# Performance work log

Hardware: AMD Instinct MI355X
Metric: run time of the kernel (lower is better)

## Reference

```python
import jax, jax.numpy as jnp
import numpy as np

IOU_THRESHOLDS = (0.5, 0.75)
B, N, G = 256, 4000, 50


def _iou(amin, amax, bmin, bmax):
    # broadcasted temporal IoU: anchors [N,1] vs boxes [1,G] -> [N,G]
    inter = jnp.maximum(jnp.minimum(amax, bmax) - jnp.maximum(amin, bmin), 0.0)
    union = (amax - amin) + (bmax - bmin) - inter
    return inter / union


def _greedy_tp(segments, gts, thr):
    # segments: [N,2], gts: [G,2]. Replicates AP.get_values greedy matching:
    # for each label (in order), claim the first (lowest-index) unused proposal
    # whose IoU > thr. Final used-mask == is_TP.
    ious = _iou(segments[:, 0:1], segments[:, 1:2], gts[None, :, 0], gts[None, :, 1])  # [N,G]
    pot = ious > thr
    n = segments.shape[0]

    def step(used, col):  # col: [N] bool, candidates for this label
        cand = col & ~used
        idx = jnp.argmax(cand)  # first True (argmax of bool is first max)
        used = jnp.where(jnp.any(cand), used.at[idx].set(True), used)
        return used, None

    used, _ = jax.lax.scan(step, jnp.zeros((n,), jnp.bool_), pot.T)
    return used  # [N] bool


def _ap_for_threshold(scores, segments, labels, thr):
    is_tp = jax.vmap(lambda s, g: _greedy_tp(s, g, thr))(segments, labels)  # [B,N]
    conf = scores.reshape(-1)                       # [B*N]
    tp = is_tp.reshape(-1).astype(jnp.float32)
    order = jnp.argsort(-conf)                      # sort by confidence, descending
    tp = tp[order]
    n_labels = labels.shape[0] * labels.shape[1]
    m = tp.shape[0]
    acc_tp = jnp.cumsum(tp)
    precision = acc_tp / (jnp.arange(m, dtype=jnp.float32) + 1.0)
    recall = acc_tp / jnp.float32(n_labels)
    # curve = [[1,0]] then (recall, precision) reversed; AP = sum(|dx| * cummax(y)[:-1])
    x = jnp.concatenate([jnp.ones((1,), jnp.float32), recall[::-1]])
    y = jnp.concatenate([jnp.zeros((1,), jnp.float32), precision[::-1]])
    y_max = jax.lax.cummax(y, axis=0)
    x_diff = jnp.abs(jnp.diff(x))
    return jnp.sum(x_diff * y_max[:-1])


def setup_inputs() -> dict:
    key = jax.random.key(0)
    k1, k2, k3, k4, k5 = jax.random.split(key, 5)
    scores = jax.random.uniform(k1, (B, N), dtype=jnp.float32)
    p_start = jax.random.uniform(k2, (B, N), dtype=jnp.float32) * 0.9
    p_len = jax.random.uniform(k3, (B, N), dtype=jnp.float32) * 0.1 + 0.005
    segments = jnp.stack([p_start, p_start + p_len], axis=-1)  # [B,N,2], start<end
    g_start = jax.random.uniform(k4, (B, G), dtype=jnp.float32) * 0.9
    g_len = jax.random.uniform(k5, (B, G), dtype=jnp.float32) * 0.1 + 0.005
    labels = jnp.stack([g_start, g_start + g_len], axis=-1)    # [B,G,2]
    return {"scores": scores, "segments": segments, "labels": labels}


def reference(scores, segments, labels):
    # returns AP at each IoU threshold, shape [len(IOU_THRESHOLDS)]
    return jnp.stack([_ap_for_threshold(scores, segments, labels, t) for t in IOU_THRESHOLDS])
```

## Files before the change

kernel.cpp:

```cpp
#include <hip/hip_runtime.h>


#define B_ 256
#define N_ 4000
#define G_ 50
#define M_ (B_ * N_)
#define NL_ (B_ * G_)
#define NBKT 2048
#define KP 16
#define TILE (NL_ / KP)

#define M0_ 0x1.000001p-1
#define M1_ 0x1.800001p-1

typedef unsigned long long u64;

__device__ __forceinline__ unsigned bucket_of(float c) {
    unsigned b = (unsigned)(c * 2048.0f);
    return b > (NBKT - 1) ? (NBKT - 1) : b;
}

__global__ __launch_bounds__(1024) void tp_kernel(
    const float* __restrict__ seg,
    const float* __restrict__ gts,
    const float* __restrict__ conf,
    int* __restrict__ tpIdx,
    int* __restrict__ cnt,
    unsigned short* __restrict__ pbh)
{
    const int tid  = threadIdx.x;
    const int lane = tid & 63;
    const int wv   = tid >> 6;
    const int b    = blockIdx.x;

    __shared__ float2 gtl[G_];
    __shared__ u64 cand[2][G_][64];
    __shared__ unsigned hls[NBKT];
    __shared__ int lcnt[2];

    #pragma unroll
    for (int k = 0; k < NBKT / 1024; ++k) hls[k * 1024 + tid] = 0u;
    if (tid < G_) gtl[tid] = ((const float2*)gts)[b * G_ + tid];
    if (tid < 2) lcnt[tid] = 0;
    __syncthreads();

    const float* cb = conf + (size_t)b * N_;
    #pragma unroll
    for (int s = 0; s < 4; ++s) {
        int n = s * 1024 + tid;
        if (n < N_) atomicAdd(&hls[bucket_of(cb[n])], 1u);
    }

    const float2* sb = (const float2*)(seg + (size_t)b * (N_ * 2));
    float pmin[4], pmax[4], plen[4];
    #pragma unroll
    for (int s = 0; s < 4; ++s) {
        int n = s * 1024 + tid;
        if (n < N_) { float2 v = sb[n]; pmin[s] = v.x; pmax[s] = v.y; }
        else { pmin[s] = 1e9f; pmax[s] = 1e9f; }
        plen[s] = pmax[s] - pmin[s];
    }
    for (int g = 0; g < G_; ++g) {
        float2 gt = gtl[g];
        float glen = gt.y - gt.x;
        u64 m0[4], m1[4];
        #pragma unroll
        for (int s = 0; s < 4; ++s) {
            float inter = fmaxf(fminf(pmax[s], gt.y) - fmaxf(pmin[s], gt.x), 0.0f);
            float uni = plen[s] + glen - inter;
            double di = (double)inter;
            double du = (double)uni;
            m0[s] = __ballot(di > M0_ * du);
            m1[s] = __ballot(di > M1_ * du);
        }
        if (lane == 0) {
            #pragma unroll
            for (int s = 0; s < 4; ++s) {
                cand[0][g][s * 16 + wv] = m0[s];
                cand[1][g][s * 16 + wv] = m1[s];
            }
        }
    }
    __syncthreads();

    #pragma unroll
    for (int k = 0; k < NBKT / 1024; ++k) {
        int bin = k * 1024 + tid;
        pbh[(size_t)b * NBKT + bin] = (unsigned short)hls[bin];
    }

    if (wv < 2) {
        const int thr_i = wv;
        u64 used = 0ull;
        for (int g = 0; g < G_; ++g) {
            u64 c = cand[thr_i][g][lane] & ~used;
            u64 ball = __ballot(c != 0ull);
            if (ball) {
                int fl = __ffsll(ball) - 1;
                if (lane == fl) used |= (c & (0ull - c));
            }
        }
        int cpop = __popcll(used);
        if (cpop) {
            int j = atomicAdd(&lcnt[thr_i], cpop);
            u64 u = used;
            while (u) {
                int bit = __ffsll(u) - 1;
                u &= u - 1;
                tpIdx[thr_i * NL_ + b * G_ + j++] = b * N_ + lane * 64 + bit;
            }
        }
    }
    __syncthreads();
    if (tid < 2) cnt[tid * B_ + b] = lcnt[tid];
}

__global__ __launch_bounds__(256) void s1_kernel(
    unsigned short* __restrict__ pbh,
    unsigned* __restrict__ total)
{
    __shared__ unsigned sc[256];
    const int bin = blockIdx.x;
    const int b = threadIdx.x;
    unsigned v = pbh[(size_t)b * NBKT + bin];
    sc[b] = v;
    __syncthreads();
    for (int off = 1; off < 256; off <<= 1) {
        unsigned add = (b >= off) ? sc[b - off] : 0u;
        __syncthreads();
        sc[b] += add;
        __syncthreads();
    }
    pbh[(size_t)b * NBKT + bin] = (unsigned short)(sc[b] - v);
    if (b == 255) total[bin] = sc[255];
}

__global__ __launch_bounds__(1024) void s2_kernel(
    const unsigned* __restrict__ total, unsigned* __restrict__ binStart)
{
    __shared__ unsigned part[1024];
    int t = threadIdx.x;
    uint2 v2 = ((const uint2*)total)[t];
    unsigned s = v2.x + v2.y;
    part[t] = s;
    __syncthreads();
    for (int off = 1; off < 1024; off <<= 1) {
        unsigned add = (t >= off) ? part[t - off] : 0u;
        __syncthreads();
        part[t] += add;
        __syncthreads();
    }
    unsigned base = (t == 0) ? 0u : part[t - 1];
    ((uint2*)binStart)[t] = make_uint2(base, base + v2.x);
}

__global__ __launch_bounds__(1024) void scatter_kernel(
    const float* __restrict__ conf,
    const unsigned short* __restrict__ pbh,
    const unsigned* __restrict__ binStart,
    u64* __restrict__ sKey)
{
    __shared__ unsigned baseB[NBKT];
    __shared__ unsigned lofs[NBKT];
    const int tid = threadIdx.x;
    const int b = blockIdx.x;
    #pragma unroll
    for (int k = 0; k < NBKT / 1024; ++k) {
        int bin = k * 1024 + tid;
        baseB[bin] = binStart[bin] + pbh[(size_t)b * NBKT + bin];
        lofs[bin] = 0u;
    }
    __syncthreads();
    const float* cb = conf + (size_t)b * N_;
    #pragma unroll
    for (int s = 0; s < 4; ++s) {
        int n = s * 1024 + tid;
        if (n < N_) {
            float c = cb[n];
            unsigned bin = bucket_of(c);
            unsigned lo = atomicAdd(&lofs[bin], 1u);
            unsigned idx = (unsigned)(b * N_ + n);
            sKey[baseB[bin] + lo] = ((u64)__float_as_uint(c) << 32) | (u64)(0xFFFFFFFFu - idx);
        }
    }
}

__global__ __launch_bounds__(256) void rank_kernel(
    const float* __restrict__ conf,
    const int* __restrict__ tpIdx,
    const int* __restrict__ cnt,
    const unsigned* __restrict__ total,
    const unsigned* __restrict__ binStart,
    const u64* __restrict__ sKey,
    int* __restrict__ tpRank)
{
    const int lane = threadIdx.x & 63;
    const int w = (blockIdx.x << 2) | (threadIdx.x >> 6);
    if (w >= 2 * NL_) return;
    const int thr_i = w / NL_;
    const int t = w - thr_i * NL_;
    const int batch = t / G_;
    const int j = t - batch * G_;

    if (j < cnt[thr_i * B_ + batch]) {
        int e = tpIdx[thr_i * NL_ + t];
        float c = conf[e];
        u64 keyE = ((u64)__float_as_uint(c) << 32) | (u64)(0xFFFFFFFFu - (unsigned)e);
        unsigned bin = bucket_of(c);
        unsigned lo = binStart[bin], n = total[bin];
        int r = M_ - (int)lo - (int)n;
        for (unsigned base = 0; base < n; base += 64) {
            unsigned k = base + lane;
            bool pred = (k < n) && (sKey[lo + k] > keyE);
            r += (int)__popcll(__ballot(pred));
        }
        if (lane == 0) tpRank[thr_i * NL_ + t] = r;
    } else {
        if (lane == 0) tpRank[thr_i * NL_ + t] = M_ + t;
    }
}

__global__ __launch_bounds__(256) void pos1_kernel(
    const int* __restrict__ tpRank,
    int* __restrict__ pcount)
{
    __shared__ alignas(16) int tile[TILE];
    const int k = blockIdx.y, thr_i = blockIdx.z;
    const int* base = tpRank + thr_i * NL_;
    for (int i = threadIdx.x; i < TILE; i += 256)
        tile[i] = base[k * TILE + i];
    __syncthreads();

    const int t0 = blockIdx.x * 1024 + threadIdx.x;
    int r[4], c[4] = {0, 0, 0, 0};
    #pragma unroll
    for (int j = 0; j < 4; ++j) {
        int t = t0 + j * 256;
        r[j] = (t < NL_) ? base[t] : -1;
    }
    const int4* l4 = (const int4*)tile;
    #pragma unroll 4
    for (int i = 0; i < TILE / 4; ++i) {
        int4 v = l4[i];
        #pragma unroll
        for (int j = 0; j < 4; ++j)
            c[j] += (v.x < r[j]) + (v.y < r[j]) + (v.z < r[j]) + (v.w < r[j]);
    }
    #pragma unroll
    for (int j = 0; j < 4; ++j) {
        int t = t0 + j * 256;
        if (t < NL_) pcount[(thr_i * KP + k) * NL_ + t] = c[j];
    }
}

__global__ __launch_bounds__(1024) void ap_kernel(
    const int* __restrict__ tpRank,
    const int* __restrict__ pcount,
    float* __restrict__ out)
{
    const int C = 13;
    __shared__ int sr[NL_];
    __shared__ float cmax[1024];
    __shared__ double red[1024];
    int thr_i = blockIdx.x;
    int t = threadIdx.x;

    #pragma unroll
    for (int j = 0; j < C; ++j) {
        int tt = t + j * 1024;
        if (tt < NL_) {
            int p = 0;
            #pragma unroll
            for (int k = 0; k < KP; ++k)
                p += pcount[(thr_i * KP + k) * NL_ + tt];
            sr[p] = tpRank[thr_i * NL_ + tt];
        }
    }
    __syncthreads();

    float pr[C]; int rk[C];
    #pragma unroll
    for (int k = 0; k < C; ++k) {
        int i = t * C + k;
        rk[k] = (i < NL_) ? sr[i] : 0x7FFFFFFF;
        pr[k] = (rk[k] < M_) ? (float)(i + 1) / (float)(rk[k] + 1) : -1.0f;
    }
    float suf[C];
    float run = -1.0f;
    #pragma unroll
    for (int k = C - 1; k >= 0; --k) { run = fmaxf(run, pr[k]); suf[k] = run; }

    cmax[t] = run;
    __syncthreads();
    for (int off = 1; off < 1024; off <<= 1) {
        float v = cmax[t];
        float o = (t + off < 1024) ? cmax[t + off] : -1.0f;
        __syncthreads();
        cmax[t] = fmaxf(v, o);
        __syncthreads();
    }
    float follow = (t + 1 < 1024) ? cmax[t + 1] : -1.0f;

    double acc = 0.0;
    #pragma unroll
    for (int k = 0; k < C; ++k) {
        int i = t * C + k;
        if (rk[k] >= 1 && rk[k] < M_) {
            float smax = fmaxf(suf[k], follow);
            float rhi = (float)(i + 1) / 12800.0f;
            float rlo = (float)i / 12800.0f;
            acc += (double)((rhi - rlo) * smax);
        }
    }
    red[t] = acc;
    __syncthreads();
    for (int off = 512; off >= 1; off >>= 1) {
        if (t < off) red[t] += red[t + off];
        __syncthreads();
    }
    if (t == 0) out[thr_i] = (float)red[0];
}

extern "C" void kernel_launch(void* const* d_in, const int* in_sizes, int n_in,
                              void* d_out, int out_size, void* d_ws, size_t ws_size,
                              hipStream_t stream) {
    const float* scores = (const float*)d_in[0];
    const float* seg    = (const float*)d_in[1];
    const float* gts    = (const float*)d_in[2];
    float* out = (float*)d_out;

    char* p = (char*)d_ws;
    int*            cnt        = (int*)p;             p += 4096;
    int*            tpIdx      = (int*)p;             p += 2 * NL_ * 4;
    int*            tpRank     = (int*)p;             p += 2 * NL_ * 4;
    unsigned*       total      = (unsigned*)p;        p += NBKT * 4;
    unsigned*       binStart   = (unsigned*)p;        p += NBKT * 4;
    unsigned short* pbh        = (unsigned short*)p;  p += (size_t)B_ * NBKT * 2;
    u64*            sKey       = (u64*)p;             p += (size_t)M_ * 8;
    int*            pcount     = (int*)sKey;
    (void)ws_size; (void)in_sizes; (void)n_in; (void)out_size;

    tp_kernel<<<B_, 1024, 0, stream>>>(seg, gts, scores, tpIdx, cnt, pbh);
    s1_kernel<<<NBKT, 256, 0, stream>>>(pbh, total);
    s2_kernel<<<1, 1024, 0, stream>>>(total, binStart);
    scatter_kernel<<<B_, 1024, 0, stream>>>(scores, pbh, binStart, sKey);
    rank_kernel<<<(2 * NL_ + 3) / 4, 256, 0, stream>>>(scores, tpIdx, cnt,
                                                       total, binStart, sKey, tpRank);
    pos1_kernel<<<dim3(13, KP, 2), 256, 0, stream>>>(tpRank, pcount);
    ap_kernel<<<2, 1024, 0, stream>>>(tpRank, pcount, out);
}
```

Before: 187.6 us.

## Fuse the seven-kernel pipeline into one cooperative kernel with grid syncs

Merges the TP-matching, histogram scan, bin-start scan, scatter, rank, position-count and AP kernels into a single cooperative mega-kernel. Grid-wide barriers replace the kernel boundaries, and shared memory is reused across phases through a union. Each block now recomputes the small bin-start scan locally instead of waiting on a separate single-block launch. This removes per-launch overhead and inter-kernel gaps. In exchange, the grid is fixed at 256 blocks of 1024 threads, so the rank and position phases loop over work with less parallelism, the position phase leaves most threads idle, and every phase pays grid.sync costs.

```diff
diff --git a/kernel.cpp b/kernel.cpp
--- a/kernel.cpp
+++ b/kernel.cpp
@@ -1,4 +1,5 @@
 #include <hip/hip_runtime.h>
+#include <hip/hip_cooperative_groups.h>
 
 
 #define B_ 256
@@ -14,311 +15,294 @@
 #define M1_ 0x1.800001p-1
 
 typedef unsigned long long u64;
+namespace cg = cooperative_groups;
 
 __device__ __forceinline__ unsigned bucket_of(float c) {
     unsigned b = (unsigned)(c * 2048.0f);
     return b > (NBKT - 1) ? (NBKT - 1) : b;
 }
 
-__global__ __launch_bounds__(1024) void tp_kernel(
-    const float* __restrict__ seg,
-    const float* __restrict__ gts,
+union SharedU {
+    struct { float2 gtl[G_]; u64 cand[2][G_][64]; unsigned hls[NBKT]; int lcnt[2]; } tp;
+    struct { unsigned sc[4][256]; } s1;
+    struct { unsigned part[1024]; unsigned baseB[NBKT]; unsigned lofs[NBKT]; } sca;
+    struct { int tile[TILE]; } pos;
+    struct { int sr[NL_]; float cmax[1024]; double red[1024]; } ap;
+};
+
+__global__ __launch_bounds__(1024, 4) void mega_kernel(
+    const float* __restrict__ seg, const float* __restrict__ gts,
     const float* __restrict__ conf,
-    int* __restrict__ tpIdx,
-    int* __restrict__ cnt,
-    unsigned short* __restrict__ pbh)
+    int* __restrict__ tpIdx, int* __restrict__ cnt,
+    unsigned short* __restrict__ pbh,
+    unsigned* __restrict__ total, unsigned* __restrict__ binStart,
+    u64* __restrict__ sKey, int* __restrict__ tpRank,
+    int* __restrict__ pcount, float* __restrict__ out)
 {
-    const int tid  = threadIdx.x;
-    const int lane = tid & 63;
-    const int wv   = tid >> 6;
-    const int b    = blockIdx.x;
-
-    __shared__ float2 gtl[G_];
-    __shared__ u64 cand[2][G_][64];
-    __shared__ unsigned hls[NBKT];
-    __shared__ int lcnt[2];
-
-    #pragma unroll
-    for (int k = 0; k < NBKT / 1024; ++k) hls[k * 1024 + tid] = 0u;
-    if (tid < G_) gtl[tid] = ((const float2*)gts)[b * G_ + tid];
-    if (tid < 2) lcnt[tid] = 0;
-    __syncthreads();
-
-    const float* cb = conf + (size_t)b * N_;
-    #pragma unroll
-    for (int s = 0; s < 4; ++s) {
-        int n = s * 1024 + tid;
-        if (n < N_) atomicAdd(&hls[bucket_of(cb[n])], 1u);
-    }
-
-    const float2* sb = (const float2*)(seg + (size_t)b * (N_ * 2));
-    float pmin[4], pmax[4], plen[4];
-    #pragma unroll
-    for (int s = 0; s < 4; ++s) {
-        int n = s * 1024 + tid;
-        if (n < N_) { float2 v = sb[n]; pmin[s] = v.x; pmax[s] = v.y; }
-        else { pmin[s] = 1e9f; pmax[s] = 1e9f; }
-        plen[s] = pmax[s] - pmin[s];
-    }
-    for (int g = 0; g < G_; ++g) {
-        float2 gt = gtl[g];
-        float glen = gt.y - gt.x;
-        u64 m0[4], m1[4];
+    cg::grid_group grid = cg::this_grid();
+    __shared__ SharedU sh;
+    const int tid = threadIdx.x, lane = tid & 63, wv = tid >> 6;
+    const int blk = blockIdx.x;
+
+    {
+        const int b = blk;
+        #pragma unroll
+        for (int k = 0; k < NBKT / 1024; ++k) sh.tp.hls[k * 1024 + tid] = 0u;
+        if (tid < G_) sh.tp.gtl[tid] = ((const float2*)gts)[b * G_ + tid];
+        if (tid < 2) sh.tp.lcnt[tid] = 0;
+        __syncthreads();
+
+        const float* cb = conf + (size_t)b * N_;
         #pragma unroll
         for (int s = 0; s < 4; ++s) {
-            float inter = fmaxf(fminf(pmax[s], gt.y) - fmaxf(pmin[s], gt.x), 0.0f);
-            float uni = plen[s] + glen - inter;
-            double di = (double)inter;
-            double du = (double)uni;
-            m0[s] = __ballot(di > M0_ * du);
-            m1[s] = __ballot(di > M1_ * du);
-        }
-        if (lane == 0) {
+            int n = s * 1024 + tid;
+            if (n < N_) atomicAdd(&sh.tp.hls[bucket_of(cb[n])], 1u);
+        }
+
+        const float2* sb = (const float2*)(seg + (size_t)b * (N_ * 2));
+        float pmin[4], pmax[4], plen[4];
+        #pragma unroll
+        for (int s = 0; s < 4; ++s) {
+            int n = s * 1024 + tid;
+            if (n < N_) { float2 v = sb[n]; pmin[s] = v.x; pmax[s] = v.y; }
+            else { pmin[s] = 1e9f; pmax[s] = 1e9f; }
+            plen[s] = pmax[s] - pmin[s];
+        }
+        for (int g = 0; g < G_; ++g) {
+            float2 gt = sh.tp.gtl[g];
+            float glen = gt.y - gt.x;
+            u64 m0[4], m1[4];
             #pragma unroll
             for (int s = 0; s < 4; ++s) {
-                cand[0][g][s * 16 + wv] = m0[s];
-                cand[1][g][s * 16 + wv] = m1[s];
-            }
-        }
-    }
-    __syncthreads();
-
-    #pragma unroll
-    for (int k = 0; k < NBKT / 1024; ++k) {
-        int bin = k * 1024 + tid;
-        pbh[(size_t)b * NBKT + bin] = (unsigned short)hls[bin];
-    }
-
-    if (wv < 2) {
-        const int thr_i = wv;
-        u64 used = 0ull;
-        for (int g = 0; g < G_; ++g) {
-            u64 c = cand[thr_i][g][lane] & ~used;
-            u64 ball = __ballot(c != 0ull);
-            if (ball) {
-                int fl = __ffsll(ball) - 1;
-                if (lane == fl) used |= (c & (0ull - c));
-            }
-        }
-        int cpop = __popcll(used);
-        if (cpop) {
-            int j = atomicAdd(&lcnt[thr_i], cpop);
-            u64 u = used;
-            while (u) {
-                int bit = __ffsll(u) - 1;
-                u &= u - 1;
-                tpIdx[thr_i * NL_ + b * G_ + j++] = b * N_ + lane * 64 + bit;
-            }
-        }
-    }
-    __syncthreads();
-    if (tid < 2) cnt[tid * B_ + b] = lcnt[tid];
-}
-
-__global__ __launch_bounds__(256) void s1_kernel(
-    unsigned short* __restrict__ pbh,
-    unsigned* __restrict__ total)
-{
-    __shared__ unsigned sc[256];
-    const int bin = blockIdx.x;
-    const int b = threadIdx.x;
-    unsigned v = pbh[(size_t)b * NBKT + bin];
-    sc[b] = v;
-    __syncthreads();
-    for (int off = 1; off < 256; off <<= 1) {
-        unsigned add = (b >= off) ? sc[b - off] : 0u;
-        __syncthreads();
-        sc[b] += add;
-        __syncthreads();
-    }
-    pbh[(size_t)b * NBKT + bin] = (unsigned short)(sc[b] - v);
-    if (b == 255) total[bin] = sc[255];
-}
-
-__global__ __launch_bounds__(1024) void s2_kernel(
-    const unsigned* __restrict__ total, unsigned* __restrict__ binStart)
-{
-    __shared__ unsigned part[1024];
-    int t = threadIdx.x;
-    uint2 v2 = ((const uint2*)total)[t];
-    unsigned s = v2.x + v2.y;
-    part[t] = s;
-    __syncthreads();
-    for (int off = 1; off < 1024; off <<= 1) {
-        unsigned add = (t >= off) ? part[t - off] : 0u;
-        __syncthreads();
-        part[t] += add;
-        __syncthreads();
-    }
-    unsigned base = (t == 0) ? 0u : part[t - 1];
-    ((uint2*)binStart)[t] = make_uint2(base, base + v2.x);
-}
-
-__global__ __launch_bounds__(1024) void scatter_kernel(
-    const float* __restrict__ conf,
-    const unsigned short* __restrict__ pbh,
-    const unsigned* __restrict__ binStart,
-    u64* __restrict__ sKey)
-{
-    __shared__ unsigned baseB[NBKT];
-    __shared__ unsigned lofs[NBKT];
-    const int tid = threadIdx.x;
-    const int b = blockIdx.x;
-    #pragma unroll
-    for (int k = 0; k < NBKT / 1024; ++k) {
-        int bin = k * 1024 + tid;
-        baseB[bin] = binStart[bin] + pbh[(size_t)b * NBKT + bin];
-        lofs[bin] = 0u;
-    }
-    __syncthreads();
-    const float* cb = conf + (size_t)b * N_;
-    #pragma unroll
-    for (int s = 0; s < 4; ++s) {
-        int n = s * 1024 + tid;
-        if (n < N_) {
-            float c = cb[n];
-            unsigned bin = bucket_of(c);
-            unsigned lo = atomicAdd(&lofs[bin], 1u);
-            unsigned idx = (unsigned)(b * N_ + n);
-            sKey[baseB[bin] + lo] = ((u64)__float_as_uint(c) << 32) | (u64)(0xFFFFFFFFu - idx);
-        }
-    }
-}
-
-__global__ __launch_bounds__(256) void rank_kernel(
-    const float* __restrict__ conf,
-    const int* __restrict__ tpIdx,
-    const int* __restrict__ cnt,
-    const unsigned* __restrict__ total,
-    const unsigned* __restrict__ binStart,
-    const u64* __restrict__ sKey,
-    int* __restrict__ tpRank)
-{
-    const int lane = threadIdx.x & 63;
-    const int w = (blockIdx.x << 2) | (threadIdx.x >> 6);
-    if (w >= 2 * NL_) return;
-    const int thr_i = w / NL_;
-    const int t = w - thr_i * NL_;
-    const int batch = t / G_;
-    const int j = t - batch * G_;
-
-    if (j < cnt[thr_i * B_ + batch]) {
-        int e = tpIdx[thr_i * NL_ + t];
-        float c = conf[e];
-        u64 keyE = ((u64)__float_as_uint(c) << 32) | (u64)(0xFFFFFFFFu - (unsigned)e);
-        unsigned bin = bucket_of(c);
-        unsigned lo = binStart[bin], n = total[bin];
-        int r = M_ - (int)lo - (int)n;
-        for (unsigned base = 0; base < n; base += 64) {
-            unsigned k = base + lane;
-            bool pred = (k < n) && (sKey[lo + k] > keyE);
-            r += (int)__popcll(__ballot(pred));
-        }
-        if (lane == 0) tpRank[thr_i * NL_ + t] = r;
-    } else {
-        if (lane == 0) tpRank[thr_i * NL_ + t] = M_ + t;
-    }
-}
-
-__global__ __launch_bounds__(256) void pos1_kernel(
-    const int* __restrict__ tpRank,
-    int* __restrict__ pcount)
-{
-    __shared__ alignas(16) int tile[TILE];
-    const int k = blockIdx.y, thr_i = blockIdx.z;
-    const int* base = tpRank + thr_i * NL_;
-    for (int i = threadIdx.x; i < TILE; i += 256)
-        tile[i] = base[k * TILE + i];
-    __syncthreads();
-
-    const int t0 = blockIdx.x * 1024 + threadIdx.x;
-    int r[4], c[4] = {0, 0, 0, 0};
-    #pragma unroll
-    for (int j = 0; j < 4; ++j) {
-        int t = t0 + j * 256;
-        r[j] = (t < NL_) ? base[t] : -1;
-    }
-    const int4* l4 = (const int4*)tile;
-    #pragma unroll 4
-    for (int i = 0; i < TILE / 4; ++i) {
-        int4 v = l4[i];
-        #pragma unroll
-        for (int j = 0; j < 4; ++j)
-            c[j] += (v.x < r[j]) + (v.y < r[j]) + (v.z < r[j]) + (v.w < r[j]);
-    }
-    #pragma unroll
-    for (int j = 0; j < 4; ++j) {
-        int t = t0 + j * 256;
-        if (t < NL_) pcount[(thr_i * KP + k) * NL_ + t] = c[j];
-    }
-}
-
-__global__ __launch_bounds__(1024) void ap_kernel(
-    const int* __restrict__ tpRank,
-    const int* __restrict__ pcount,
-    float* __restrict__ out)
-{
-    const int C = 13;
-    __shared__ int sr[NL_];
-    __shared__ float cmax[1024];
-    __shared__ double red[1024];
-    int thr_i = blockIdx.x;
-    int t = threadIdx.x;
-
-    #pragma unroll
-    for (int j = 0; j < C; ++j) {
-        int tt = t + j * 1024;
-        if (tt < NL_) {
-            int p = 0;
-            #pragma unroll
-            for (int k = 0; k < KP; ++k)
-                p += pcount[(thr_i * KP + k) * NL_ + tt];
-            sr[p] = tpRank[thr_i * NL_ + tt];
-        }
-    }
-    __syncthreads();
-
-    float pr[C]; int rk[C];
-    #pragma unroll
-    for (int k = 0; k < C; ++k) {
-        int i = t * C + k;
-        rk[k] = (i < NL_) ? sr[i] : 0x7FFFFFFF;
-        pr[k] = (rk[k] < M_) ? (float)(i + 1) / (float)(rk[k] + 1) : -1.0f;
-    }
-    float suf[C];
-    float run = -1.0f;
-    #pragma unroll
-    for (int k = C - 1; k >= 0; --k) { run = fmaxf(run, pr[k]); suf[k] = run; }
-
-    cmax[t] = run;
-    __syncthreads();
-    for (int off = 1; off < 1024; off <<= 1) {
-        float v = cmax[t];
-        float o = (t + off < 1024) ? cmax[t + off] : -1.0f;
-        __syncthreads();
-        cmax[t] = fmaxf(v, o);
-        __syncthreads();
-    }
-    float follow = (t + 1 < 1024) ? cmax[t + 1] : -1.0f;
-
-    double acc = 0.0;
-    #pragma unroll
-    for (int k = 0; k < C; ++k) {
-        int i = t * C + k;
-        if (rk[k] >= 1 && rk[k] < M_) {
-            float smax = fmaxf(suf[k], follow);
-            float rhi = (float)(i + 1) / 12800.0f;
-            float rlo = (float)i / 12800.0f;
-            acc += (double)((rhi - rlo) * smax);
-        }
-    }
-    red[t] = acc;
-    __syncthreads();
-    for (int off = 512; off >= 1; off >>= 1) {
-        if (t < off) red[t] += red[t + off];
-        __syncthreads();
-    }
-    if (t == 0) out[thr_i] = (float)red[0];
+                float inter = fmaxf(fminf(pmax[s], gt.y) - fmaxf(pmin[s], gt.x), 0.0f);
+                float uni = plen[s] + glen - inter;
+                double di = (double)inter;
+                double du = (double)uni;
+                m0[s] = __ballot(di > M0_ * du);
+                m1[s] = __ballot(di > M1_ * du);
+            }
+            if (lane == 0) {
+                #pragma unroll
+                for (int s = 0; s < 4; ++s) {
+                    sh.tp.cand[0][g][s * 16 + wv] = m0[s];
+                    sh.tp.cand[1][g][s * 16 + wv] = m1[s];
+                }
+            }
+        }
+        __syncthreads();
+
+        #pragma unroll
+        for (int k = 0; k < NBKT / 1024; ++k) {
+            int bin = k * 1024 + tid;
+            pbh[(size_t)b * NBKT + bin] = (unsigned short)sh.tp.hls[bin];
+        }
+
+        if (wv < 2) {
+            const int thr_i = wv;
+            u64 used = 0ull;
+            for (int g = 0; g < G_; ++g) {
+                u64 c = sh.tp.cand[thr_i][g][lane] & ~used;
+                u64 ball = __ballot(c != 0ull);
+                if (ball) {
+                    int fl = __ffsll(ball) - 1;
+                    if (lane == fl) used |= (c & (0ull - c));
+                }
+            }
+            int cpop = __popcll(used);
+            if (cpop) {
+                int j = atomicAdd(&sh.tp.lcnt[thr_i], cpop);
+                u64 u = used;
+                while (u) {
+                    int bit = __ffsll(u) - 1;
+                    u &= u - 1;
+                    tpIdx[thr_i * NL_ + b * G_ + j++] = b * N_ + lane * 64 + bit;
+                }
+            }
+        }
+        __syncthreads();
+        if (tid < 2) cnt[tid * B_ + b] = sh.tp.lcnt[tid];
+    }
+    grid.sync();
+
+    {
+        const int grp = tid >> 8;
+        const int b = tid & 255;
+        for (int r = 0; r < 2; ++r) {
+            int bin = blk * 8 + r * 4 + grp;
+            unsigned v = pbh[(size_t)b * NBKT + bin];
+            sh.s1.sc[grp][b] = v;
+            __syncthreads();
+            for (int off = 1; off < 256; off <<= 1) {
+                unsigned add = (b >= off) ? sh.s1.sc[grp][b - off] : 0u;
+                __syncthreads();
+                sh.s1.sc[grp][b] += add;
+                __syncthreads();
+            }
+            pbh[(size_t)b * NBKT + bin] = (unsigned short)(sh.s1.sc[grp][b] - v);
+            if (b == 255) total[bin] = sh.s1.sc[grp][255];
+            __syncthreads();
+        }
+    }
+    grid.sync();
+
+    {
+        uint2 v2 = ((const uint2*)total)[tid];
+        unsigned s = v2.x + v2.y;
+        sh.sca.part[tid] = s;
+        __syncthreads();
+        for (int off = 1; off < 1024; off <<= 1) {
+            unsigned add = (tid >= off) ? sh.sca.part[tid - off] : 0u;
+            __syncthreads();
+            sh.sca.part[tid] += add;
+            __syncthreads();
+        }
+        unsigned base = tid ? sh.sca.part[tid - 1] : 0u;
+        if (blk == 0) ((uint2*)binStart)[tid] = make_uint2(base, base + v2.x);
+        const int b = blk;
+        sh.sca.baseB[2 * tid]     = base        + pbh[(size_t)b * NBKT + 2 * tid];
+        sh.sca.baseB[2 * tid + 1] = base + v2.x + pbh[(size_t)b * NBKT + 2 * tid + 1];
+        sh.sca.lofs[2 * tid] = 0u;
+        sh.sca.lofs[2 * tid + 1] = 0u;
+        __syncthreads();
+        const float* cb = conf + (size_t)b * N_;
+        #pragma unroll
+        for (int s4 = 0; s4 < 4; ++s4) {
+            int n = s4 * 1024 + tid;
+            if (n < N_) {
+                float c = cb[n];
+                unsigned bin = bucket_of(c);
+                unsigned lo = atomicAdd(&sh.sca.lofs[bin], 1u);
+                unsigned idx = (unsigned)(b * N_ + n);
+                sKey[sh.sca.baseB[bin] + lo] =
+                    ((u64)__float_as_uint(c) << 32) | (u64)(0xFFFFFFFFu - idx);
+            }
+        }
+    }
+    grid.sync();
+
+    {
+        const int gw = blk * 16 + wv;
+        for (int t = gw; t < 2 * NL_; t += 4096) {
+            const int thr_i = t / NL_;
+            const int tt = t - thr_i * NL_;
+            const int batch = tt / G_;
+            const int j = tt - batch * G_;
+            if (j < cnt[thr_i * B_ + batch]) {
+                int e = tpIdx[thr_i * NL_ + tt];
+                float c = conf[e];
+                u64 keyE = ((u64)__float_as_uint(c) << 32) | (u64)(0xFFFFFFFFu - (unsigned)e);
+                unsigned bin = bucket_of(c);
+                unsigned lo = binStart[bin], n = total[bin];
+                int r = M_ - (int)lo - (int)n;
+                for (unsigned base = 0; base < n; base += 64) {
+                    unsigned k = base + lane;
+                    bool pred = (k < n) && (sKey[lo + k] > keyE);
+                    r += (int)__popcll(__ballot(pred));
+                }
+                if (lane == 0) tpRank[thr_i * NL_ + tt] = r;
+            } else {
+                if (lane == 0) tpRank[thr_i * NL_ + tt] = M_ + t % NL_ + thr_i;
+            }
+        }
+    }
+    grid.sync();
+
+    {
+        for (int task = blk; task < 2 * KP * 13; task += B_) {
+            int xb = task % 13;
+            int rem = task / 13;
+            int k = rem % KP;
+            int thr_i = rem / KP;
+            const int* baseR = tpRank + thr_i * NL_;
+            for (int i = tid; i < TILE; i += 1024)
+                sh.pos.tile[i] = baseR[k * TILE + i];
+            __syncthreads();
+            if (tid < 256) {
+                const int t0 = xb * 1024 + tid;
+                int r[4], c[4] = {0, 0, 0, 0};
+                #pragma unroll
+                for (int j = 0; j < 4; ++j) {
+                    int t = t0 + j * 256;
+                    r[j] = (t < NL_) ? baseR[t] : -1;
+                }
+                const int4* l4 = (const int4*)sh.pos.tile;
+                #pragma unroll 4
+                for (int i = 0; i < TILE / 4; ++i) {
+                    int4 v = l4[i];
+                    #pragma unroll
+                    for (int j = 0; j < 4; ++j)
+                        c[j] += (v.x < r[j]) + (v.y < r[j]) + (v.z < r[j]) + (v.w < r[j]);
+                }
+                #pragma unroll
+                for (int j = 0; j < 4; ++j) {
+                    int t = t0 + j * 256;
+                    if (t < NL_) pcount[(thr_i * KP + k) * NL_ + t] = c[j];
+                }
+            }
+            __syncthreads();
+        }
+    }
+    grid.sync();
+
+    if (blk < 2) {
+        const int C = 13;
+        const int thr_i = blk;
+        const int t = tid;
+        #pragma unroll
+        for (int j = 0; j < C; ++j) {
+            int tt = t + j * 1024;
+            if (tt < NL_) {
+                int p = 0;
+                #pragma unroll
+                for (int k = 0; k < KP; ++k)
+                    p += pcount[(thr_i * KP + k) * NL_ + tt];
+                sh.ap.sr[p] = tpRank[thr_i * NL_ + tt];
+            }
+        }
+        __syncthreads();
+
+        float pr[C]; int rk[C];
+        #pragma unroll
+        for (int k = 0; k < C; ++k) {
+            int i = t * C + k;
+            rk[k] = (i < NL_) ? sh.ap.sr[i] : 0x7FFFFFFF;
+            pr[k] = (rk[k] < M_) ? (float)(i + 1) / (float)(rk[k] + 1) : -1.0f;
+        }
+        float suf[C];
+        float run = -1.0f;
+        #pragma unroll
+        for (int k = C - 1; k >= 0; --k) { run = fmaxf(run, pr[k]); suf[k] = run; }
+
+        sh.ap.cmax[t] = run;
+        __syncthreads();
+        for (int off = 1; off < 1024; off <<= 1) {
+            float v = sh.ap.cmax[t];
+            float o = (t + off < 1024) ? sh.ap.cmax[t + off] : -1.0f;
+            __syncthreads();
+            sh.ap.cmax[t] = fmaxf(v, o);
+            __syncthreads();
+        }
+        float follow = (t + 1 < 1024) ? sh.ap.cmax[t + 1] : -1.0f;
+
+        double acc = 0.0;
+        #pragma unroll
+        for (int k = 0; k < C; ++k) {
+            int i = t * C + k;
+            if (rk[k] >= 1 && rk[k] < M_) {
+                float smax = fmaxf(suf[k], follow);
+                float rhi = (float)(i + 1) / 12800.0f;
+                float rlo = (float)i / 12800.0f;
+                acc += (double)((rhi - rlo) * smax);
+            }
+        }
+        sh.ap.red[t] = acc;
+        __syncthreads();
+        for (int off = 512; off >= 1; off >>= 1) {
+            if (t < off) sh.ap.red[t] += sh.ap.red[t + off];
+            __syncthreads();
+        }
+        if (t == 0) out[thr_i] = (float)sh.ap.red[0];
+    }
 }
 
 extern "C" void kernel_launch(void* const* d_in, const int* in_sizes, int n_in,
@@ -340,12 +324,12 @@
     int*            pcount     = (int*)sKey;
     (void)ws_size; (void)in_sizes; (void)n_in; (void)out_size;
 
-    tp_kernel<<<B_, 1024, 0, stream>>>(seg, gts, scores, tpIdx, cnt, pbh);
-    s1_kernel<<<NBKT, 256, 0, stream>>>(pbh, total);
-    s2_kernel<<<1, 1024, 0, stream>>>(total, binStart);
-    scatter_kernel<<<B_, 1024, 0, stream>>>(scores, pbh, binStart, sKey);
-    rank_kernel<<<(2 * NL_ + 3) / 4, 256, 0, stream>>>(scores, tpIdx, cnt,
-                                                       total, binStart, sKey, tpRank);
-    pos1_kernel<<<dim3(13, KP, 2), 256, 0, stream>>>(tpRank, pcount);
-    ap_kernel<<<2, 1024, 0, stream>>>(tpRank, pcount, out);
+    void* args[] = {
+        (void*)&seg, (void*)&gts, (void*)&scores,
+        (void*)&tpIdx, (void*)&cnt, (void*)&pbh,
+        (void*)&total, (void*)&binStart,
+        (void*)&sKey, (void*)&tpRank, (void*)&pcount, (void*)&out
+    };
+    hipLaunchCooperativeKernel((const void*)mega_kernel, dim3(B_), dim3(1024),
+                               args, 0, stream);
 }
```

New measurement: 354.3 us. +88.9%, slower.

## Fold bin-start scan into scatter kernel and use wave shuffles in s1

Applied to the files above, without the earlier changes.

Removes the single-block s2 launch: each scatter block now recomputes the global exclusive scan of bucket totals in shared memory, and block 0 writes binStart for later kernels. The s1 per-bin scan across batches becomes a wave-level shuffle scan with four bins per block and four batches per lane, replacing the shared-memory scan with many barriers. KP is also halved, changing the tiling of pos1. This trades one kernel launch and a serial dependency for redundant scan work in every scatter block.

```diff
diff --git a/kernel.cpp b/kernel.cpp
--- a/kernel.cpp
+++ b/kernel.cpp
@@ -7,7 +7,7 @@
 #define M_ (B_ * N_)
 #define NL_ (B_ * G_)
 #define NBKT 2048
-#define KP 16
+#define KP 8
 #define TILE (NL_ / KP)
 
 #define M0_ 0x1.000001p-1
@@ -119,62 +119,62 @@
     unsigned short* __restrict__ pbh,
     unsigned* __restrict__ total)
 {
-    __shared__ unsigned sc[256];
-    const int bin = blockIdx.x;
-    const int b = threadIdx.x;
-    unsigned v = pbh[(size_t)b * NBKT + bin];
-    sc[b] = v;
-    __syncthreads();
-    for (int off = 1; off < 256; off <<= 1) {
-        unsigned add = (b >= off) ? sc[b - off] : 0u;
-        __syncthreads();
-        sc[b] += add;
-        __syncthreads();
-    }
-    pbh[(size_t)b * NBKT + bin] = (unsigned short)(sc[b] - v);
-    if (b == 255) total[bin] = sc[255];
-}
-
-__global__ __launch_bounds__(1024) void s2_kernel(
-    const unsigned* __restrict__ total, unsigned* __restrict__ binStart)
-{
-    __shared__ unsigned part[1024];
-    int t = threadIdx.x;
-    uint2 v2 = ((const uint2*)total)[t];
-    unsigned s = v2.x + v2.y;
-    part[t] = s;
-    __syncthreads();
-    for (int off = 1; off < 1024; off <<= 1) {
-        unsigned add = (t >= off) ? part[t - off] : 0u;
-        __syncthreads();
-        part[t] += add;
-        __syncthreads();
-    }
-    unsigned base = (t == 0) ? 0u : part[t - 1];
-    ((uint2*)binStart)[t] = make_uint2(base, base + v2.x);
+    const int lane = threadIdx.x & 63;
+    const int bin = blockIdx.x * 4 + (threadIdx.x >> 6);
+    unsigned v[4], loc[4], s = 0;
+    #pragma unroll
+    for (int i = 0; i < 4; ++i) {
+        v[i] = pbh[(size_t)(lane * 4 + i) * NBKT + bin];
+        loc[i] = s; s += v[i];
+    }
+    unsigned x = s;
+    #pragma unroll
+    for (int off = 1; off < 64; off <<= 1) {
+        unsigned t = __shfl_up(x, off, 64);
+        if (lane >= off) x += t;
+    }
+    unsigned excl = x - s;
+    #pragma unroll
+    for (int i = 0; i < 4; ++i)
+        pbh[(size_t)(lane * 4 + i) * NBKT + bin] = (unsigned short)(excl + loc[i]);
+    if (lane == 63) total[bin] = x;
 }
 
 __global__ __launch_bounds__(1024) void scatter_kernel(
     const float* __restrict__ conf,
     const unsigned short* __restrict__ pbh,
-    const unsigned* __restrict__ binStart,
+    const unsigned* __restrict__ total,
+    unsigned* __restrict__ binStart,
     u64* __restrict__ sKey)
 {
+    __shared__ unsigned part[1024];
     __shared__ unsigned baseB[NBKT];
     __shared__ unsigned lofs[NBKT];
     const int tid = threadIdx.x;
     const int b = blockIdx.x;
-    #pragma unroll
-    for (int k = 0; k < NBKT / 1024; ++k) {
-        int bin = k * 1024 + tid;
-        baseB[bin] = binStart[bin] + pbh[(size_t)b * NBKT + bin];
-        lofs[bin] = 0u;
-    }
-    __syncthreads();
+
+    uint2 v2 = ((const uint2*)total)[tid];
+    unsigned s = v2.x + v2.y;
+    part[tid] = s;
+    __syncthreads();
+    for (int off = 1; off < 1024; off <<= 1) {
+        unsigned add = (tid >= off) ? part[tid - off] : 0u;
+        __syncthreads();
+        part[tid] += add;
+        __syncthreads();
+    }
+    unsigned base = tid ? part[tid - 1] : 0u;
+    if (b == 0) ((uint2*)binStart)[tid] = make_uint2(base, base + v2.x);
+    baseB[2 * tid]     = base        + pbh[(size_t)b * NBKT + 2 * tid];
+    baseB[2 * tid + 1] = base + v2.x + pbh[(size_t)b * NBKT + 2 * tid + 1];
+    lofs[2 * tid] = 0u;
+    lofs[2 * tid + 1] = 0u;
+    __syncthreads();
+
     const float* cb = conf + (size_t)b * N_;
     #pragma unroll
-    for (int s = 0; s < 4; ++s) {
-        int n = s * 1024 + tid;
+    for (int s4 = 0; s4 < 4; ++s4) {
+        int n = s4 * 1024 + tid;
         if (n < N_) {
             float c = cb[n];
             unsigned bin = bucket_of(c);
@@ -341,9 +341,8 @@
     (void)ws_size; (void)in_sizes; (void)n_in; (void)out_size;
 
     tp_kernel<<<B_, 1024, 0, stream>>>(seg, gts, scores, tpIdx, cnt, pbh);
-    s1_kernel<<<NBKT, 256, 0, stream>>>(pbh, total);
-    s2_kernel<<<1, 1024, 0, stream>>>(total, binStart);
-    scatter_kernel<<<B_, 1024, 0, stream>>>(scores, pbh, binStart, sKey);
+    s1_kernel<<<NBKT / 4, 256, 0, stream>>>(pbh, total);
+    scatter_kernel<<<B_, 1024, 0, stream>>>(scores, pbh, total, binStart, sKey);
     rank_kernel<<<(2 * NL_ + 3) / 4, 256, 0, stream>>>(scores, tpIdx, cnt,
                                                        total, binStart, sKey, tpRank);
     pos1_kernel<<<dim3(13, KP, 2), 256, 0, stream>>>(tpRank, pcount);
```

Result: no change. 188.3 us (+0.4%).
